# Performance work log

Hardware: AMD Instinct MI355X
Metric: run time of the kernel (lower is better)

Reference implementation:

```python
import jax, jax.numpy as jnp
import numpy as np

N_NODES = 100000
N_EDGES = 1600000   # avg in-degree 16
D_IN = 128
D_HID = 256
N_CLASSES = 40
N_GRAPHS = 64


def setup_inputs() -> dict:
    key = jax.random.key(0)
    ks = jax.random.split(key, 8)
    h = jax.random.normal(ks[0], (N_NODES, D_IN), dtype=jnp.float32)
    src = jax.random.randint(ks[1], (N_EDGES,), 0, N_NODES, dtype=jnp.int64)
    dst = jax.random.randint(ks[2], (N_EDGES,), 0, N_NODES, dtype=jnp.int64)
    graph_ids = jnp.sort(jax.random.randint(ks[3], (N_NODES,), 0, N_GRAPHS, dtype=jnp.int64))
    s_in = 1.0 / np.sqrt(D_IN)
    s_hid = 1.0 / np.sqrt(D_HID)
    W_self = jax.random.uniform(ks[4], (D_IN, D_HID), jnp.float32, -s_in, s_in)
    W_neigh = jax.random.uniform(ks[5], (D_IN, D_HID), jnp.float32, -s_in, s_in)
    b = jnp.zeros((D_HID,), jnp.float32)
    W_pred = jax.random.uniform(ks[6], (D_HID, N_CLASSES), jnp.float32, -s_hid, s_hid)
    b_pred = jnp.zeros((N_CLASSES,), jnp.float32)
    return {"h": h, "W_self": W_self, "W_neigh": W_neigh, "b": b,
            "W_pred": W_pred, "b_pred": b_pred,
            "src": src, "dst": dst, "graph_ids": graph_ids}


def reference(h, W_self, W_neigh, b, W_pred, b_pred, src, dst, graph_ids):
    n_nodes = h.shape[0]
    # --- SAGEConv 'mean': mean over in-neighbors (gather src feats, scatter-add to dst) ---
    deg = jax.ops.segment_sum(jnp.ones_like(dst, dtype=h.dtype), dst, num_segments=n_nodes)
    agg = jax.ops.segment_sum(h[src], dst, num_segments=n_nodes)  # [N, D_IN]
    h_neigh = agg / jnp.maximum(deg, 1.0)[:, None]  # zero-in-degree -> 0
    hid = jax.nn.relu(h @ W_self + h_neigh @ W_neigh + b)  # [N, D_HID]
    # --- AvgPooling per graph ---
    cnt = jax.ops.segment_sum(jnp.ones((n_nodes,), h.dtype), graph_ids, num_segments=N_GRAPHS)
    pooled = jax.ops.segment_sum(hid, graph_ids, num_segments=N_GRAPHS) / jnp.maximum(cnt, 1.0)[:, None]
    # --- prediction head (dropout is identity in eval) ---
    return pooled @ W_pred + b_pred  # [N_GRAPHS, N_CLASSES]
```

## Files before the change

### kernel.cpp

```cpp
#include <hip/hip_runtime.h>
#include <stdint.h>

constexpr int kNodes    = 100000;
constexpr int kEdges    = 1600000;
constexpr int kDin      = 128;
constexpr int kK        = 256;
constexpr int kDhid     = 256;
constexpr int kClasses  = 40;
constexpr int kGraphs   = 64;

constexpr int kBktShift = 8;
constexpr int NB = (kNodes + 255) >> 8;
constexpr int kBktCap = 5120;
constexpr int kChunk = 6250;
constexpr int kEBlocks = (kEdges + kChunk - 1) / kChunk;
constexpr int kCvtBlocks = (kNodes * 32 + kK * kDhid) / 256;

constexpr int kTPB = 5;
constexpr int kTiles = kNodes / 32;
constexpr int kGemmBlocks = kTiles / kTPB;

typedef __attribute__((ext_vector_type(8))) short bf8_t;
typedef __attribute__((ext_vector_type(4))) float f4_t;
typedef __attribute__((ext_vector_type(2))) float f2_t;

__device__ inline ushort f2bf(float f) {
  uint32_t u = __float_as_uint(f);
  u += 0x7fff + ((u >> 16) & 1);
  return (ushort)(u >> 16);
}

template <bool HI>
__device__ inline f2_t fp8x2_f32(uint32_t w) {
#if __has_builtin(__builtin_amdgcn_cvt_pk_f32_fp8)
  return __builtin_amdgcn_cvt_pk_f32_fp8(w, HI);
#else
  f2_t r;
  uint32_t b0 = HI ? ((w >> 16) & 0xffu) : (w & 0xffu);
  uint32_t b1 = HI ? (w >> 24) : ((w >> 8) & 0xffu);
  auto dec = [](uint32_t b) -> float {
    uint32_t s = (b & 0x80u) << 24;
    uint32_t em = b & 0x7fu;
    float mag;
    if (em >= 0x08u) {
      uint32_t e = (em >> 3) - 7 + 127;
      mag = __uint_as_float((e << 23) | ((em & 7u) << 20));
    } else {
      mag = (float)em * 0.001953125f;
    }
    return __uint_as_float(s | __float_as_uint(mag));
  };
  r.x = dec(b0); r.y = dec(b1);
  return r;
#endif
}

__device__ inline uint32_t f32_to_e4m3(float f) {
  uint32_t sgn = (__float_as_uint(f) >> 31) << 7;
  float mag = fabsf(f);
  uint32_t r;
  if (mag >= 0.015625f) {
    uint32_t u = __float_as_uint(mag);
    u += 0x7FFFF + ((u >> 20) & 1);
    int e = (int)(u >> 23) - 127;
    if (e > 8) r = 0x7Eu;
    else r = (uint32_t)((e + 7) << 3) | ((u >> 20) & 7u);
  } else {
    float m = mag * 512.f;
    int mi = (int)rintf(m);
    r = (mi > 7) ? 0x08u : (uint32_t)mi;
  }
  return r | sgn;
}

__device__ inline uint32_t pack4_e4m3(float x, float y, float z, float w) {
#if __has_builtin(__builtin_amdgcn_cvt_pk_fp8_f32)
  uint32_t p = __builtin_amdgcn_cvt_pk_fp8_f32(x, y, 0u, false);
  return __builtin_amdgcn_cvt_pk_fp8_f32(z, w, p, true);
#else
  return f32_to_e4m3(x) | (f32_to_e4m3(y) << 8) |
         (f32_to_e4m3(z) << 16) | (f32_to_e4m3(w) << 24);
#endif
}

__global__ void bucket_scatter(const int* __restrict__ src, const int* __restrict__ dst,
                               int* __restrict__ bktCur, uint32_t* __restrict__ pairs) {
  __shared__ int hist[NB], base[NB], cur[NB];
  for (int i = threadIdx.x; i < NB; i += 256) { hist[i] = 0; cur[i] = 0; }
  __syncthreads();
  int e0 = blockIdx.x * kChunk;
  int e1 = min(e0 + kChunk, kEdges);
  for (int e = e0 + threadIdx.x; e < e1; e += 256)
    atomicAdd(&hist[dst[e] >> kBktShift], 1);
  __syncthreads();
  for (int i = threadIdx.x; i < NB; i += 256)
    base[i] = hist[i] ? atomicAdd(&bktCur[i], hist[i]) : 0;
  __syncthreads();
  for (int e = e0 + threadIdx.x; e < e1; e += 256) {
    int d = dst[e];
    int b = d >> kBktShift;
    int p = atomicAdd(&cur[b], 1);
    pairs[(size_t)b * kBktCap + base[b] + p] = ((uint32_t)src[e] << 8) | (uint32_t)(d & 255);
  }
}

__global__ void fill_cvt(const uint32_t* __restrict__ pairs, const int* __restrict__ bktCur,
                         int* __restrict__ row, int* __restrict__ rend, int* __restrict__ csr,
                         const float* __restrict__ h, const float* __restrict__ Ws,
                         const float* __restrict__ Wn, ushort* __restrict__ A16,
                         ushort* __restrict__ Wt, uint8_t* __restrict__ H8,
                         int fillBlocks) {
  __shared__ int deg[256], scn[256], cur[256];
  if ((int)blockIdx.x < fillBlocks) {
    int b = blockIdx.x;
    int t = threadIdx.x;
    int cnt = bktCur[b];
    int e0 = b * kBktCap;
    int nb0 = b << kBktShift;
    deg[t] = 0;
    __syncthreads();
    for (int e = t; e < cnt; e += 256)
      atomicAdd(&deg[pairs[e0 + e] & 255u], 1);
    __syncthreads();
    int d = deg[t];
    scn[t] = d;
    __syncthreads();
#pragma unroll
    for (int off = 1; off < 256; off <<= 1) {
      int u = (t >= off) ? scn[t - off] : 0;
      __syncthreads();
      scn[t] += u;
      __syncthreads();
    }
    int excl = scn[t] - d;
    cur[t] = excl;
    int n = nb0 + t;
    if (n < kNodes) { row[n] = e0 + excl; rend[n] = e0 + scn[t]; }
    __syncthreads();
    for (int e = t; e < cnt; e += 256) {
      uint32_t pr = pairs[e0 + e];
      int p = atomicAdd(&cur[pr & 255u], 1);
      csr[e0 + p] = (int)(pr >> 8);
    }
  } else {
    int t = ((int)blockIdx.x - fillBlocks) * 256 + threadIdx.x;
    const int hN = kNodes * 32;
    if (t < hN) {
      int n = t >> 5;
      int c4 = (t & 31) * 4;
      float4 v = *reinterpret_cast<const float4*>(h + (size_t)n * kDin + c4);
      ushort4 o;
      o.x = f2bf(v.x); o.y = f2bf(v.y); o.z = f2bf(v.z); o.w = f2bf(v.w);
      *reinterpret_cast<ushort4*>(A16 + (size_t)n * kK + c4) = o;
      *reinterpret_cast<uint32_t*>(H8 + (size_t)n * kDin + c4) =
          pack4_e4m3(v.x, v.y, v.z, v.w);
    } else {
      int u = t - hN;
      int j = u & 255;
      int k = u >> 8;
      float v = (k < 128) ? Ws[(size_t)k * kDhid + j] : Wn[(size_t)(k - 128) * kDhid + j];
      Wt[(size_t)j * kK + k] = f2bf(v);
    }
  }
}

__global__ void aggregate8(const uint8_t* __restrict__ H8, ushort* __restrict__ A16,
                           const int* __restrict__ row, const int* __restrict__ rend,
                           const int* __restrict__ csr) {
  int wv = (blockIdx.x * 256 + threadIdx.x) >> 6;
  int lane = threadIdx.x & 63;
  int grp = lane >> 4;
  int sub = lane & 15;
  int n = wv * 4 + grp;
  int s0 = row[n], s1 = rend[n];
  float a0 = 0.f, a1 = 0.f, a2 = 0.f, a3 = 0.f, a4 = 0.f, a5 = 0.f, a6 = 0.f, a7 = 0.f;
#pragma unroll 4
  for (int i = s0; i < s1; ++i) {
    int s = csr[i];
    uint2 v = *reinterpret_cast<const uint2*>(H8 + (size_t)s * kDin + sub * 8);
    f2_t l0 = fp8x2_f32<false>(v.x), h0 = fp8x2_f32<true>(v.x);
    f2_t l1 = fp8x2_f32<false>(v.y), h1 = fp8x2_f32<true>(v.y);
    a0 += l0.x; a1 += l0.y; a2 += h0.x; a3 += h0.y;
    a4 += l1.x; a5 += l1.y; a6 += h1.x; a7 += h1.y;
  }
  float rd = 1.f / fmaxf((float)(s1 - s0), 1.f);
  uint4 o;
  o.x = (uint32_t)f2bf(a0 * rd) | ((uint32_t)f2bf(a1 * rd) << 16);
  o.y = (uint32_t)f2bf(a2 * rd) | ((uint32_t)f2bf(a3 * rd) << 16);
  o.z = (uint32_t)f2bf(a4 * rd) | ((uint32_t)f2bf(a5 * rd) << 16);
  o.w = (uint32_t)f2bf(a6 * rd) | ((uint32_t)f2bf(a7 * rd) << 16);
  *reinterpret_cast<uint4*>((char*)A16 + (size_t)n * 512 + 256 + sub * 16) = o;
}

__global__ __launch_bounds__(256, 2)
void gemm_pool(const ushort* __restrict__ A16, const ushort* __restrict__ Wt,
               const float* __restrict__ bias, const int* __restrict__ gid,
               float* __restrict__ gsum) {
  __shared__ ushort Abuf[2][32 * 256];
  const int tid  = threadIdx.x;
  const int lane = tid & 63;
  const int wave = tid >> 6;
  const int lhi = lane >> 4;
  const int llo = lane & 15;

  bf8_t bfr[4][8];
#pragma unroll
  for (int nf = 0; nf < 4; ++nf) {
    const char* wrow = (const char*)Wt + (size_t)(wave * 64 + nf * 16 + llo) * 512 + lhi * 16;
#pragma unroll
    for (int kk = 0; kk < 8; ++kk)
      bfr[nf][kk] = *reinterpret_cast<const bf8_t*>(wrow + kk * 64);
  }
  float bv[4];
#pragma unroll
  for (int nf = 0; nf < 4; ++nf) bv[nf] = bias[wave * 64 + nf * 16 + llo];

  auto stage = [&](int buf, int tile) {
#pragma unroll
    for (int i = 0; i < 4; ++i) {
      int r = i * 8 + (tid >> 5);
      int wb = (tid & 31) * 16;
      size_t gsrc = ((size_t)tile * 32 + r) * 512 + (size_t)(wb ^ ((r & 7) << 4));
      uint32_t ldst = (uint32_t)(i * 4096 + tid * 16);
      __builtin_amdgcn_global_load_lds(
          (const __attribute__((address_space(1))) uint32_t*)((const char*)A16 + gsrc),
          (__attribute__((address_space(3))) uint32_t*)((char*)&Abuf[buf][0] + ldst),
          16, 0, 0);
    }
  };

  const int t0 = blockIdx.x * kTPB;
  stage(0, t0);
  __syncthreads();

  float pooled[4] = {0.f, 0.f, 0.f, 0.f};
  int cur_g = gid[t0 * 32];

  for (int ti = 0; ti < kTPB; ++ti) {
    int tile = t0 + ti;
    if (ti + 1 < kTPB) stage((ti + 1) & 1, tile + 1);

    f4_t acc[2][4];
#pragma unroll
    for (int mf = 0; mf < 2; ++mf)
#pragma unroll
      for (int nf = 0; nf < 4; ++nf) acc[mf][nf] = (f4_t)0.f;
    const char* abase = (const char*)&Abuf[ti & 1][0];
    const int swz = (llo & 7) << 4;
#pragma unroll
    for (int kk = 0; kk < 8; ++kk) {
      int kb = kk * 64 + lhi * 16;
      bf8_t x0 = *reinterpret_cast<const bf8_t*>(abase + llo * 512 + (kb ^ swz));
      bf8_t x1 = *reinterpret_cast<const bf8_t*>(abase + (16 + llo) * 512 + (kb ^ swz));
#pragma unroll
      for (int nf = 0; nf < 4; ++nf) {
        acc[0][nf] = __builtin_amdgcn_mfma_f32_16x16x32_bf16(x0, bfr[nf][kk], acc[0][nf], 0, 0, 0);
        acc[1][nf] = __builtin_amdgcn_mfma_f32_16x16x32_bf16(x1, bfr[nf][kk], acc[1][nf], 0, 0, 0);
      }
    }

    int base = tile * 32;
    int gA = gid[base], gB = gid[base + 31];
    if (gA == gB) {
      if (gA != cur_g) {
#pragma unroll
        for (int nf = 0; nf < 4; ++nf) {
          if (pooled[nf] != 0.f)
            atomicAdd(&gsum[cur_g * kDhid + wave * 64 + nf * 16 + llo], pooled[nf]);
          pooled[nf] = 0.f;
        }
        cur_g = gA;
      }
#pragma unroll
      for (int nf = 0; nf < 4; ++nf) {
        float s = 0.f;
#pragma unroll
        for (int mf = 0; mf < 2; ++mf)
#pragma unroll
          for (int q = 0; q < 4; ++q) s += fmaxf(acc[mf][nf][q] + bv[nf], 0.f);
        pooled[nf] += s;
      }
    } else {
#pragma unroll
      for (int mf = 0; mf < 2; ++mf)
#pragma unroll
        for (int q = 0; q < 4; ++q) {
          int r = base + mf * 16 + lhi * 4 + q;
          int g = gid[r];
#pragma unroll
          for (int nf = 0; nf < 4; ++nf) {
            float v = fmaxf(acc[mf][nf][q] + bv[nf], 0.f);
            if (v != 0.f) atomicAdd(&gsum[g * kDhid + wave * 64 + nf * 16 + llo], v);
          }
        }
    }
    __syncthreads();
  }

#pragma unroll
  for (int nf = 0; nf < 4; ++nf)
    if (pooled[nf] != 0.f)
      atomicAdd(&gsum[cur_g * kDhid + wave * 64 + nf * 16 + llo], pooled[nf]);
}

__global__ void head_kernel(const float* __restrict__ gsum,
                            const float* __restrict__ Wp,
                            const float* __restrict__ bp,
                            const int* __restrict__ gid,
                            float* __restrict__ out) {
  int g = blockIdx.x;
  int c = threadIdx.x;
  int lo0 = 0, hi0 = kNodes;
  while (lo0 < hi0) { int m = (lo0 + hi0) >> 1; if (gid[m] < g) lo0 = m + 1; else hi0 = m; }
  int lo1 = lo0, hi1 = kNodes;
  while (lo1 < hi1) { int m = (lo1 + hi1) >> 1; if (gid[m] < g + 1) lo1 = m + 1; else hi1 = m; }
  float rc = 1.0f / fmaxf((float)(lo1 - lo0), 1.0f);
  if (c < kClasses) {
    float acc = bp[c];
    for (int k = 0; k < kDhid; ++k)
      acc += gsum[g * kDhid + k] * rc * Wp[k * kClasses + c];
    out[g * kClasses + c] = acc;
  }
}

extern "C" void kernel_launch(void* const* d_in, const int* in_sizes, int n_in,
                              void* d_out, int out_size, void* d_ws, size_t ws_size,
                              hipStream_t stream) {
  const float* h  = (const float*)d_in[0];
  const float* Ws = (const float*)d_in[1];
  const float* Wn = (const float*)d_in[2];
  const float* b  = (const float*)d_in[3];
  const float* Wp = (const float*)d_in[4];
  const float* bp = (const float*)d_in[5];
  const int* src  = (const int*)d_in[6];
  const int* dst  = (const int*)d_in[7];
  const int* gid  = (const int*)d_in[8];
  float* out = (float*)d_out;

  char* ws = (char*)d_ws;
  const size_t a16Off    = 0;
  const size_t wtOff     = 51249152;
  const size_t csrOff    = 51380224;
  const size_t rowOff    = 59408384;
  const size_t rendOff   = 59808384;
  const size_t gsumOff   = 60208384;
  const size_t bktCurOff = 60273920;
  const size_t h8Off     = 60275712;
  const size_t pairsOff  = 73075712;
  const size_t needBig   = pairsOff + 8028160;
  ushort* A16     = (ushort*)(ws + a16Off);
  ushort* Wt      = (ushort*)(ws + wtOff);
  int* csr        = (int*)(ws + csrOff);
  int* row        = (int*)(ws + rowOff);
  int* rend       = (int*)(ws + rendOff);
  float* gsum     = (float*)(ws + gsumOff);
  int* bktCur     = (int*)(ws + bktCurOff);
  uint8_t* H8     = (uint8_t*)(ws + h8Off);
  const bool bigWs = (ws_size >= needBig);
  uint32_t* pairs = bigWs ? (uint32_t*)(ws + pairsOff) : (uint32_t*)(ws + a16Off);

  (void)hipMemsetAsync(ws + gsumOff, 0, (60273920 + 1568) - 60208384, stream);

  hipLaunchKernelGGL(bucket_scatter, dim3(kEBlocks), dim3(256), 0, stream, src, dst, bktCur, pairs);

  if (bigWs) {
    hipLaunchKernelGGL(fill_cvt, dim3(NB + kCvtBlocks), dim3(256), 0, stream,
                       pairs, bktCur, row, rend, csr, h, Ws, Wn, A16, Wt, H8, NB);
  } else {
    hipLaunchKernelGGL(fill_cvt, dim3(NB), dim3(256), 0, stream,
                       pairs, bktCur, row, rend, csr, h, Ws, Wn, A16, Wt, H8, NB);
    hipLaunchKernelGGL(fill_cvt, dim3(kCvtBlocks), dim3(256), 0, stream,
                       pairs, bktCur, row, rend, csr, h, Ws, Wn, A16, Wt, H8, 0);
  }

  hipLaunchKernelGGL(aggregate8, dim3(kNodes / 16), dim3(256), 0, stream,
                     H8, A16, row, rend, csr);

  hipLaunchKernelGGL(gemm_pool, dim3(kGemmBlocks), dim3(256), 0, stream,
                     A16, Wt, b, gid, gsum);
  hipLaunchKernelGGL(head_kernel, dim3(kGraphs), dim3(64), 0, stream,
                     gsum, Wp, bp, gid, out);
}
```

Baseline: 145.8 us.

## Fuse edge bucket scatter with feature conversion and retune GEMM blocking

Moves the h/W conversion work from the fill kernel into the bucket-scatter launch, so conversion blocks run concurrently with the edge scatter and the bucket fill becomes a small separate kernel. Edge chunks shrink so the scatter uses more blocks. The GEMM uses fewer tiles per block, with tail handling, and a higher occupancy hint in launch bounds, which may cost registers or spill given the preloaded weight fragments. Smaller scatter chunks also increase the number of global atomics on bucket counters.

```diff
diff --git a/kernel.cpp b/kernel.cpp
--- a/kernel.cpp
+++ b/kernel.cpp
@@ -12,13 +12,13 @@
 constexpr int kBktShift = 8;
 constexpr int NB = (kNodes + 255) >> 8;
 constexpr int kBktCap = 5120;
-constexpr int kChunk = 6250;
-constexpr int kEBlocks = (kEdges + kChunk - 1) / kChunk;
+constexpr int kChunk = 1600;
+constexpr int kEBlocks = kEdges / kChunk;
 constexpr int kCvtBlocks = (kNodes * 32 + kK * kDhid) / 256;
 
-constexpr int kTPB = 5;
+constexpr int kTPB = 3;
 constexpr int kTiles = kNodes / 32;
-constexpr int kGemmBlocks = kTiles / kTPB;
+constexpr int kGemmBlocks = (kTiles + kTPB - 1) / kTPB;
 
 typedef __attribute__((ext_vector_type(8))) short bf8_t;
 typedef __attribute__((ext_vector_type(4))) float f4_t;
@@ -83,67 +83,32 @@
 #endif
 }
 
-__global__ void bucket_scatter(const int* __restrict__ src, const int* __restrict__ dst,
-                               int* __restrict__ bktCur, uint32_t* __restrict__ pairs) {
+__global__ void scatter_cvt(const int* __restrict__ src, const int* __restrict__ dst,
+                            int* __restrict__ bktCur, uint32_t* __restrict__ pairs,
+                            const float* __restrict__ h, const float* __restrict__ Ws,
+                            const float* __restrict__ Wn, ushort* __restrict__ A16,
+                            ushort* __restrict__ Wt, uint8_t* __restrict__ H8,
+                            int scatterBlocks) {
   __shared__ int hist[NB], base[NB], cur[NB];
-  for (int i = threadIdx.x; i < NB; i += 256) { hist[i] = 0; cur[i] = 0; }
-  __syncthreads();
-  int e0 = blockIdx.x * kChunk;
-  int e1 = min(e0 + kChunk, kEdges);
-  for (int e = e0 + threadIdx.x; e < e1; e += 256)
-    atomicAdd(&hist[dst[e] >> kBktShift], 1);
-  __syncthreads();
-  for (int i = threadIdx.x; i < NB; i += 256)
-    base[i] = hist[i] ? atomicAdd(&bktCur[i], hist[i]) : 0;
-  __syncthreads();
-  for (int e = e0 + threadIdx.x; e < e1; e += 256) {
-    int d = dst[e];
-    int b = d >> kBktShift;
-    int p = atomicAdd(&cur[b], 1);
-    pairs[(size_t)b * kBktCap + base[b] + p] = ((uint32_t)src[e] << 8) | (uint32_t)(d & 255);
-  }
-}
-
-__global__ void fill_cvt(const uint32_t* __restrict__ pairs, const int* __restrict__ bktCur,
-                         int* __restrict__ row, int* __restrict__ rend, int* __restrict__ csr,
-                         const float* __restrict__ h, const float* __restrict__ Ws,
-                         const float* __restrict__ Wn, ushort* __restrict__ A16,
-                         ushort* __restrict__ Wt, uint8_t* __restrict__ H8,
-                         int fillBlocks) {
-  __shared__ int deg[256], scn[256], cur[256];
-  if ((int)blockIdx.x < fillBlocks) {
-    int b = blockIdx.x;
-    int t = threadIdx.x;
-    int cnt = bktCur[b];
-    int e0 = b * kBktCap;
-    int nb0 = b << kBktShift;
-    deg[t] = 0;
-    __syncthreads();
-    for (int e = t; e < cnt; e += 256)
-      atomicAdd(&deg[pairs[e0 + e] & 255u], 1);
-    __syncthreads();
-    int d = deg[t];
-    scn[t] = d;
-    __syncthreads();
-#pragma unroll
-    for (int off = 1; off < 256; off <<= 1) {
-      int u = (t >= off) ? scn[t - off] : 0;
-      __syncthreads();
-      scn[t] += u;
-      __syncthreads();
-    }
-    int excl = scn[t] - d;
-    cur[t] = excl;
-    int n = nb0 + t;
-    if (n < kNodes) { row[n] = e0 + excl; rend[n] = e0 + scn[t]; }
-    __syncthreads();
-    for (int e = t; e < cnt; e += 256) {
-      uint32_t pr = pairs[e0 + e];
-      int p = atomicAdd(&cur[pr & 255u], 1);
-      csr[e0 + p] = (int)(pr >> 8);
+  if ((int)blockIdx.x < scatterBlocks) {
+    for (int i = threadIdx.x; i < NB; i += 256) { hist[i] = 0; cur[i] = 0; }
+    __syncthreads();
+    int e0 = blockIdx.x * kChunk;
+    int e1 = min(e0 + kChunk, kEdges);
+    for (int e = e0 + threadIdx.x; e < e1; e += 256)
+      atomicAdd(&hist[dst[e] >> kBktShift], 1);
+    __syncthreads();
+    for (int i = threadIdx.x; i < NB; i += 256)
+      base[i] = hist[i] ? atomicAdd(&bktCur[i], hist[i]) : 0;
+    __syncthreads();
+    for (int e = e0 + threadIdx.x; e < e1; e += 256) {
+      int d = dst[e];
+      int b = d >> kBktShift;
+      int p = atomicAdd(&cur[b], 1);
+      pairs[(size_t)b * kBktCap + base[b] + p] = ((uint32_t)src[e] << 8) | (uint32_t)(d & 255);
     }
   } else {
-    int t = ((int)blockIdx.x - fillBlocks) * 256 + threadIdx.x;
+    int t = ((int)blockIdx.x - scatterBlocks) * 256 + threadIdx.x;
     const int hN = kNodes * 32;
     if (t < hN) {
       int n = t >> 5;
@@ -161,6 +126,42 @@
       float v = (k < 128) ? Ws[(size_t)k * kDhid + j] : Wn[(size_t)(k - 128) * kDhid + j];
       Wt[(size_t)j * kK + k] = f2bf(v);
     }
+  }
+}
+
+__global__ void bucket_fill(const uint32_t* __restrict__ pairs, const int* __restrict__ bktCur,
+                            int* __restrict__ row, int* __restrict__ rend,
+                            int* __restrict__ csr) {
+  __shared__ int deg[256], scn[256], cur[256];
+  int b = blockIdx.x;
+  int t = threadIdx.x;
+  int cnt = bktCur[b];
+  int e0 = b * kBktCap;
+  int nb0 = b << kBktShift;
+  deg[t] = 0;
+  __syncthreads();
+  for (int e = t; e < cnt; e += 256)
+    atomicAdd(&deg[pairs[e0 + e] & 255u], 1);
+  __syncthreads();
+  int d = deg[t];
+  scn[t] = d;
+  __syncthreads();
+#pragma unroll
+  for (int off = 1; off < 256; off <<= 1) {
+    int u = (t >= off) ? scn[t - off] : 0;
+    __syncthreads();
+    scn[t] += u;
+    __syncthreads();
+  }
+  int excl = scn[t] - d;
+  cur[t] = excl;
+  int n = nb0 + t;
+  if (n < kNodes) { row[n] = e0 + excl; rend[n] = e0 + scn[t]; }
+  __syncthreads();
+  for (int e = t; e < cnt; e += 256) {
+    uint32_t pr = pairs[e0 + e];
+    int p = atomicAdd(&cur[pr & 255u], 1);
+    csr[e0 + p] = (int)(pr >> 8);
   }
 }
 
@@ -192,7 +193,7 @@
   *reinterpret_cast<uint4*>((char*)A16 + (size_t)n * 512 + 256 + sub * 16) = o;
 }
 
-__global__ __launch_bounds__(256, 2)
+__global__ __launch_bounds__(256, 4)
 void gemm_pool(const ushort* __restrict__ A16, const ushort* __restrict__ Wt,
                const float* __restrict__ bias, const int* __restrict__ gid,
                float* __restrict__ gsum) {
@@ -230,15 +231,16 @@
   };
 
   const int t0 = blockIdx.x * kTPB;
+  const int nt = min(kTPB, kTiles - t0);
   stage(0, t0);
   __syncthreads();
 
   float pooled[4] = {0.f, 0.f, 0.f, 0.f};
   int cur_g = gid[t0 * 32];
 
-  for (int ti = 0; ti < kTPB; ++ti) {
+  for (int ti = 0; ti < nt; ++ti) {
     int tile = t0 + ti;
-    if (ti + 1 < kTPB) stage((ti + 1) & 1, tile + 1);
+    if (ti + 1 < nt) stage((ti + 1) & 1, tile + 1);
 
     f4_t acc[2][4];
 #pragma unroll
@@ -361,16 +363,18 @@
 
   (void)hipMemsetAsync(ws + gsumOff, 0, (60273920 + 1568) - 60208384, stream);
 
-  hipLaunchKernelGGL(bucket_scatter, dim3(kEBlocks), dim3(256), 0, stream, src, dst, bktCur, pairs);
-
   if (bigWs) {
-    hipLaunchKernelGGL(fill_cvt, dim3(NB + kCvtBlocks), dim3(256), 0, stream,
-                       pairs, bktCur, row, rend, csr, h, Ws, Wn, A16, Wt, H8, NB);
+    hipLaunchKernelGGL(scatter_cvt, dim3(kEBlocks + kCvtBlocks), dim3(256), 0, stream,
+                       src, dst, bktCur, pairs, h, Ws, Wn, A16, Wt, H8, kEBlocks);
+    hipLaunchKernelGGL(bucket_fill, dim3(NB), dim3(256), 0, stream,
+                       pairs, bktCur, row, rend, csr);
   } else {
-    hipLaunchKernelGGL(fill_cvt, dim3(NB), dim3(256), 0, stream,
-                       pairs, bktCur, row, rend, csr, h, Ws, Wn, A16, Wt, H8, NB);
-    hipLaunchKernelGGL(fill_cvt, dim3(kCvtBlocks), dim3(256), 0, stream,
-                       pairs, bktCur, row, rend, csr, h, Ws, Wn, A16, Wt, H8, 0);
+    hipLaunchKernelGGL(scatter_cvt, dim3(kEBlocks), dim3(256), 0, stream,
+                       src, dst, bktCur, pairs, h, Ws, Wn, A16, Wt, H8, kEBlocks);
+    hipLaunchKernelGGL(bucket_fill, dim3(NB), dim3(256), 0, stream,
+                       pairs, bktCur, row, rend, csr);
+    hipLaunchKernelGGL(scatter_cvt, dim3(kCvtBlocks), dim3(256), 0, stream,
+                       src, dst, bktCur, pairs, h, Ws, Wn, A16, Wt, H8, 0);
   }
 
   hipLaunchKernelGGL(aggregate8, dim3(kNodes / 16), dim3(256), 0, stream,
```

Result: slower. 221.1 us (+51.6%).
